# Kernel optimization log

Hardware: AMD Instinct MI355X
Metric: run time of the kernel (lower is better)

Reference implementation:

```python
import jax, jax.numpy as jnp
import numpy as np

V_NODES = 50000


def _spmm(vals, rows, cols, m):
    # sparse (V,V) @ dense (V, F): gather source rows, scale, scatter-add to dest rows
    return jax.ops.segment_sum(vals[:, None] * m[cols], rows, num_segments=V_NODES)


def setup_inputs() -> dict:
    key = jax.random.key(0)
    ks = jax.random.split(key, 6)
    B, Cin, Cout, K, V, E = 4, 128, 128, 5, V_NODES, 800000
    x = jax.random.normal(ks[0], (B, Cin, V), dtype=jnp.float32)
    # random symmetric-normalized-laplacian-like values (scaled so recurrence stays bounded)
    lap_vals = jax.random.normal(ks[1], (E,), dtype=jnp.float32) * 0.05
    fan_in = Cin  # kaiming_normal_ mode='fan_in' on (K, Cin, Cout): fan_in = Cin
    weight = jax.random.normal(ks[2], (K, Cin, Cout), dtype=jnp.float32) * np.sqrt(2.0 / fan_in)
    bias = jnp.full((Cout,), 0.01, dtype=jnp.float32)
    lap_rows = jax.random.randint(ks[3], (E,), 0, V, dtype=jnp.int32)
    lap_cols = jax.random.randint(ks[4], (E,), 0, V, dtype=jnp.int32)
    return {"x": x, "lap_vals": lap_vals, "weight": weight, "bias": bias,
            "lap_rows": lap_rows, "lap_cols": lap_cols}


def reference(x, lap_vals, weight, bias, lap_rows, lap_cols):
    B, Cin, V = x.shape
    K, _, Cout = weight.shape
    # (B, Cin, V) -> (V, B*Cin)
    x0 = jnp.transpose(x, (2, 0, 1)).reshape(V, B * Cin)

    def contract(xk, k):
        # accumulate order-k contribution: (V, B, Cin) x (Cin, Cout) -> (V, B, Cout)
        return jnp.einsum('vbi,io->vbo', xk.reshape(V, B, Cin), weight[k])

    out = contract(x0, 0)
    if K > 1:
        x1 = _spmm(lap_vals, lap_rows, lap_cols, x0)
        out = out + contract(x1, 1)
        for k in range(2, K):
            x2 = 2.0 * _spmm(lap_vals, lap_rows, lap_cols, x1) - x0
            out = out + contract(x2, k)
            x0, x1 = x1, x2
    out = out + bias  # broadcast over (V, B, Cout)
    # (V, B, Cout) -> (B, Cout, V)
    return jnp.transpose(out, (1, 2, 0))
```

## Files before the change

### kernel.cpp

```cpp
#include <hip/hip_runtime.h>

#define V_NODES 50000
#define FDIM    512
#define CIN     128
#define COUT    128
#define BATCH   4
#define KORD    5
#define KTOT    (KORD * CIN)
#define SCAN_NBLK ((V_NODES + 255) / 256)
#define TR_BLOCKS (((V_NODES + 63) / 64) * (FDIM / 64))
#define CONVW_BLOCKS ((KORD * COUT + 3) / 4)
#define QUANT_BLOCKS ((V_NODES + 3) / 4)

typedef short s16x8 __attribute__((ext_vector_type(8)));
typedef float f32x4 __attribute__((ext_vector_type(4)));
typedef int   i32x4 __attribute__((ext_vector_type(4)));

struct EPair { float w; int c; };

__device__ __forceinline__ float bf2f(unsigned short u) {
    union { unsigned int i; float f; } x; x.i = ((unsigned int)u) << 16; return x.f;
}
__device__ __forceinline__ unsigned short f2bf(float f) {
    union { float f; unsigned int i; } x; x.f = f;
    unsigned int r = x.i + 0x7fffu + ((x.i >> 16) & 1u);
    return (unsigned short)(r >> 16);
}

__global__ __launch_bounds__(256) void prep1_kernel(const float* __restrict__ x,
                                                    unsigned short* __restrict__ t0,
                                                    const int* __restrict__ rows,
                                                    int* __restrict__ cnt,
                                                    int E, int histBlocks,
                                                    const float* __restrict__ W,
                                                    signed char* __restrict__ Wq8,
                                                    float* __restrict__ Wsc) {
    __shared__ float tile[64][65];
    const int bid = blockIdx.x;
    if (bid < TR_BLOCKS) {
        const int v0 = (bid % ((V_NODES + 63) / 64)) * 64;
        const int r0 = (bid / ((V_NODES + 63) / 64)) * 64;
        const int lane = threadIdx.x & 63;
        const int w = threadIdx.x >> 6;
        #pragma unroll
        for (int i = 0; i < 16; ++i) {
            int rr = w * 16 + i;
            int v = v0 + lane;
            tile[rr][lane] = (v < V_NODES) ? x[(size_t)(r0 + rr) * V_NODES + v] : 0.0f;
        }
        __syncthreads();
        #pragma unroll
        for (int i = 0; i < 16; ++i) {
            int vv = w * 16 + i;
            int v = v0 + vv;
            if (v < V_NODES) t0[(size_t)v * FDIM + r0 + lane] = f2bf(tile[lane][vv]);
        }
    } else if (bid < TR_BLOCKS + histBlocks) {
        int e = (bid - TR_BLOCKS) * 256 + threadIdx.x;
        if (e < E) atomicAdd(&cnt[rows[e]], 1);
    } else {
        const int g = (bid - TR_BLOCKS - histBlocks) * 4 + (threadIdx.x >> 6);
        if (g >= KORD * COUT) return;
        const int co = g & 127;
        const int ord = g >> 7;
        const int lane = threadIdx.x & 63;
        float w0 = W[(size_t)(ord * 128 + lane * 2 + 0) * COUT + co];
        float w1 = W[(size_t)(ord * 128 + lane * 2 + 1) * COUT + co];
        float m = fmaxf(fabsf(w0), fabsf(w1));
        #pragma unroll
        for (int off = 1; off < 64; off <<= 1) m = fmaxf(m, __shfl_xor(m, off, 64));
        float inv = (m > 0.f) ? 127.f / m : 0.f;
        int q0 = max(-127, min(127, (int)rintf(w0 * inv)));
        int q1 = max(-127, min(127, (int)rintf(w1 * inv)));
        unsigned short pk = (unsigned short)((q0 & 0xff) | ((q1 & 0xff) << 8));
        *(unsigned short*)(Wq8 + (size_t)co * KTOT + ord * 128 + lane * 2) = pk;
        if (lane == 0) Wsc[ord * 128 + co] = m / 127.f;
    }
}

__global__ __launch_bounds__(256) void scan1_kernel(const int* __restrict__ cnt,
                                                    int* __restrict__ rowPtr,
                                                    int* __restrict__ blkSum) {
    __shared__ int sh[256];
    const int t = threadIdx.x;
    const int i = blockIdx.x * 256 + t;
    int v = (i < V_NODES) ? cnt[i] : 0;
    sh[t] = v;
    __syncthreads();
    #pragma unroll
    for (int off = 1; off < 256; off <<= 1) {
        int u = (t >= off) ? sh[t - off] : 0;
        __syncthreads();
        sh[t] += u;
        __syncthreads();
    }
    if (i < V_NODES) rowPtr[i] = sh[t] - v;
    if (t == 255) blkSum[blockIdx.x] = sh[255];
}

__global__ __launch_bounds__(256) void scan23_kernel(const int* __restrict__ blkSum,
                                                     int* __restrict__ rowPtr,
                                                     int* __restrict__ cursor) {
    __shared__ int sh[256];
    const int t = threadIdx.x;
    int v = (t < SCAN_NBLK) ? blkSum[t] : 0;
    sh[t] = v;
    __syncthreads();
    #pragma unroll
    for (int off = 1; off < 256; off <<= 1) {
        int u = (t >= off) ? sh[t - off] : 0;
        __syncthreads();
        sh[t] += u;
        __syncthreads();
    }
    const int boff = sh[blockIdx.x] - blkSum[blockIdx.x];
    const int i = blockIdx.x * 256 + t;
    if (i < V_NODES) {
        int r = rowPtr[i] + boff;
        rowPtr[i] = r;
        cursor[i] = r;
    }
    if (blockIdx.x == 0 && t == 255) rowPtr[V_NODES] = sh[255];
}

__global__ __launch_bounds__(256) void prep2_kernel(const unsigned short* __restrict__ xb,
                                                    signed char* __restrict__ xi,
                                                    float* __restrict__ xs,
                                                    const float* __restrict__ vals,
                                                    const int* __restrict__ rows,
                                                    const int* __restrict__ cols,
                                                    int* __restrict__ cursor,
                                                    EPair* __restrict__ ep, int E) {
    const int bid = blockIdx.x;
    if (bid < QUANT_BLOCKS) {
        const int wid = threadIdx.x >> 6;
        const int lane = threadIdx.x & 63;
        const int row = bid * 4 + wid;
        if (row >= V_NODES) return;
        uint4 q = ((const uint4*)xb)[(size_t)row * 64 + lane];
        unsigned int u[4] = {q.x, q.y, q.z, q.w};
        float f[8];
        #pragma unroll
        for (int j = 0; j < 4; ++j) {
            f[2*j+0] = bf2f((unsigned short)(u[j] & 0xffffu));
            f[2*j+1] = bf2f((unsigned short)(u[j] >> 16));
        }
        float m = 0.f;
        #pragma unroll
        for (int j = 0; j < 8; ++j) m = fmaxf(m, fabsf(f[j]));
        #pragma unroll
        for (int off = 1; off < 64; off <<= 1) m = fmaxf(m, __shfl_xor(m, off, 64));
        float inv = (m > 0.f) ? 127.f / m : 0.f;
        uint2 o; unsigned int ow[2] = {0u, 0u};
        #pragma unroll
        for (int j = 0; j < 8; ++j) {
            int si = (int)rintf(f[j] * inv);
            si = max(-127, min(127, si));
            ow[j >> 2] |= ((unsigned int)(si & 0xff)) << (8 * (j & 3));
        }
        o.x = ow[0]; o.y = ow[1];
        ((uint2*)xi)[(size_t)row * 64 + lane] = o;
        if (lane == 0) xs[row] = m / 127.f;
    } else {
        int e = (bid - QUANT_BLOCKS) * 256 + threadIdx.x;
        if (e >= E) return;
        int r = rows[e];
        int pos = atomicAdd(&cursor[r], 1);
        EPair p; p.w = vals[e]; p.c = cols[e];
        ep[pos] = p;
    }
}

__global__ __launch_bounds__(256) void spmm_i8_kernel(const EPair* __restrict__ ep,
                                                      const int* __restrict__ rowPtr,
                                                      const signed char* __restrict__ xi,
                                                      const float* __restrict__ xsc,
                                                      const signed char* __restrict__ oldi,
                                                      const float* __restrict__ oldsc,
                                                      signed char* __restrict__ yi,
                                                      float* __restrict__ ysc,
                                                      float alpha, int beta) {
    const int wid = threadIdx.x >> 6;
    const int lane = threadIdx.x & 63;
    const int row = blockIdx.x * 4 + wid;
    if (row >= V_NODES) return;
    const int s = rowPtr[row], e_end = rowPtr[row + 1];
    const uint2* __restrict__ xq = (const uint2*)xi;

    float acc[8];
    #pragma unroll
    for (int j = 0; j < 8; ++j) acc[j] = 0.f;

    int e = s;
    for (; e + 3 < e_end; e += 4) {
        EPair p[4];
        #pragma unroll
        for (int i = 0; i < 4; ++i) p[i] = ep[e + i];
        float w[4];
        #pragma unroll
        for (int i = 0; i < 4; ++i) w[i] = p[i].w * xsc[p[i].c];
        uint2 q[4];
        #pragma unroll
        for (int i = 0; i < 4; ++i) q[i] = xq[(size_t)p[i].c * 64 + lane];
        #pragma unroll
        for (int i = 0; i < 4; ++i) {
            #pragma unroll
            for (int wd = 0; wd < 2; ++wd) {
                unsigned int uu = wd ? q[i].y : q[i].x;
                #pragma unroll
                for (int b = 0; b < 4; ++b) {
                    float xv = (float)((signed char)(uu >> (8 * b)));
                    acc[wd * 4 + b] += w[i] * xv;
                }
            }
        }
    }
    for (; e < e_end; ++e) {
        EPair p0 = ep[e];
        float w0 = p0.w * xsc[p0.c];
        uint2 q0 = xq[(size_t)p0.c * 64 + lane];
        #pragma unroll
        for (int wd = 0; wd < 2; ++wd) {
            unsigned int uu = wd ? q0.y : q0.x;
            #pragma unroll
            for (int b = 0; b < 4; ++b) {
                float xv = (float)((signed char)(uu >> (8 * b)));
                acc[wd * 4 + b] += w0 * xv;
            }
        }
    }

    float r[8];
    #pragma unroll
    for (int j = 0; j < 8; ++j) r[j] = alpha * acc[j];
    if (beta) {
        uint2 q = ((const uint2*)oldi)[(size_t)row * 64 + lane];
        const float os = oldsc[row];
        #pragma unroll
        for (int wd = 0; wd < 2; ++wd) {
            unsigned int uu = wd ? q.y : q.x;
            #pragma unroll
            for (int b = 0; b < 4; ++b)
                r[wd * 4 + b] -= os * (float)((signed char)(uu >> (8 * b)));
        }
    }

    float m = 0.f;
    #pragma unroll
    for (int j = 0; j < 8; ++j) m = fmaxf(m, fabsf(r[j]));
    #pragma unroll
    for (int off = 1; off < 64; off <<= 1) m = fmaxf(m, __shfl_xor(m, off, 64));
    float inv = (m > 0.f) ? 127.f / m : 0.f;
    unsigned int ow[2] = {0u, 0u};
    #pragma unroll
    for (int j = 0; j < 8; ++j) {
        int si = (int)rintf(r[j] * inv);
        si = max(-127, min(127, si));
        ow[j >> 2] |= ((unsigned int)(si & 0xff)) << (8 * (j & 3));
    }
    uint2 oi; oi.x = ow[0]; oi.y = ow[1];
    ((uint2*)yi)[(size_t)row * 64 + lane] = oi;
    if (lane == 0) ysc[row] = m / 127.f;
}

__global__ __launch_bounds__(512) void gemm_mfma_kernel(const signed char* __restrict__ Ti8,
                                                        const float* __restrict__ Tsc,
                                                        const signed char* __restrict__ Wq8,
                                                        const float* __restrict__ Wsc,
                                                        const float* __restrict__ bias,
                                                        float* __restrict__ out) {
    __shared__ signed char Abuf[3][128 * 64];
    const int tid = threadIdx.x;
    const int lane = tid & 63;
    const int wid = tid >> 6;
    const int wr = wid >> 2;
    const int wc = wid & 3;
    const int v0 = blockIdx.x * 128;
    const int b = blockIdx.y;
    const int lr = lane & 15;
    const int lk = lane >> 4;

    size_t gof;
    {
        int rl = tid >> 2;
        int ch = tid & 3;
        int rowg = v0 + rl;
        if (rowg >= V_NODES) rowg = V_NODES - 1;
        int srcch = (ch - ((rl >> 1) & 3)) & 3;
        gof = (size_t)rowg * FDIM + b * CIN + (size_t)(srcch << 4);
    }

    f32x4 accF[4][2];
    i32x4 accI[4][2];
    #pragma unroll
    for (int mf = 0; mf < 4; ++mf)
        #pragma unroll
        for (int nf = 0; nf < 2; ++nf) {
            accF[mf][nf] = (f32x4){0.f, 0.f, 0.f, 0.f};
            accI[mf][nf] = (i32x4){0, 0, 0, 0};
        }

    const signed char* Bb = Wq8 + (size_t)(wc * 32 + lr) * KTOT + lk * 16;

    #pragma unroll
    for (int st = 0; st < 2; ++st) {
        const size_t soff = (size_t)(st & 1) * 64;
        __builtin_amdgcn_global_load_lds(
            (const __attribute__((address_space(1))) void*)(Ti8 + gof + soff),
            (__attribute__((address_space(3))) void*)(&Abuf[st][tid * 16]),
            16, 0, 0);
    }
    i32x4 bcur[2];
    #pragma unroll
    for (int nf = 0; nf < 2; ++nf)
        bcur[nf] = *(const i32x4*)(Bb + (size_t)nf * 16 * KTOT);
    f32x4 sv[4];
    float swv0 = 0.f, swv1 = 0.f;
    asm volatile("s_waitcnt vmcnt(0)" ::: "memory");
    asm volatile("s_barrier" ::: "memory");

    int curm = 0, stm = 2;
    #pragma unroll 1
    for (int s = 0; s < 10; ++s) {
        i32x4 bnxt[2];
        if (s < 9) {
            #pragma unroll
            for (int nf = 0; nf < 2; ++nf)
                bnxt[nf] = *(const i32x4*)(Bb + (size_t)nf * 16 * KTOT + (s + 1) * 64);
        }
        if (!(s & 1)) {
            const int ord = s >> 1;
            #pragma unroll
            for (int mf = 0; mf < 4; ++mf) {
                int base = v0 + wr * 64 + mf * 16 + lk * 4;
                if (base > V_NODES - 4) base = V_NODES - 4;
                sv[mf] = *(const f32x4*)(Tsc + (size_t)ord * V_NODES + base);
            }
            swv0 = Wsc[ord * 128 + wc * 32 + lr];
            swv1 = Wsc[ord * 128 + wc * 32 + 16 + lr];
        }
        __builtin_amdgcn_sched_barrier(0);
        if (s < 8) {
            const int sn = s + 2;
            const size_t soff = (size_t)(sn >> 1) * ((size_t)V_NODES * FDIM) + (size_t)((sn & 1) * 64);
            __builtin_amdgcn_global_load_lds(
                (const __attribute__((address_space(1))) void*)(Ti8 + gof + soff),
                (__attribute__((address_space(3))) void*)(&Abuf[stm][tid * 16]),
                16, 0, 0);
        }
        const signed char* Ab = &Abuf[curm][0];
        i32x4 a[4];
        #pragma unroll
        for (int mf = 0; mf < 4; ++mf) {
            int rl = wr * 64 + mf * 16 + lr;
            int phys = rl * 64 + (((lk + (rl >> 1)) & 3) << 4);
            a[mf] = *(const i32x4*)(Ab + phys);
        }
        #pragma unroll
        for (int mf = 0; mf < 4; ++mf)
            #pragma unroll
            for (int nf = 0; nf < 2; ++nf)
                accI[mf][nf] = __builtin_amdgcn_mfma_i32_16x16x64_i8(a[mf], bcur[nf], accI[mf][nf], 0, 0, 0);
        if (s & 1) {
            #pragma unroll
            for (int mf = 0; mf < 4; ++mf)
                #pragma unroll
                for (int nf = 0; nf < 2; ++nf) {
                    float sw = nf ? swv1 : swv0;
                    #pragma unroll
                    for (int e = 0; e < 4; ++e)
                        accF[mf][nf][e] += (float)accI[mf][nf][e] * (sv[mf][e] * sw);
                    accI[mf][nf] = (i32x4){0, 0, 0, 0};
                }
        }
        if (s < 9) {
            bcur[0] = bnxt[0];
            bcur[1] = bnxt[1];
        }
        asm volatile("s_barrier" ::: "memory");
        curm = (curm == 2) ? 0 : curm + 1;
        stm  = (stm == 2) ? 0 : stm + 1;
    }

    float* lds_f = (float*)&Abuf[0][0];
    const float bs0 = bias[wc * 32 + lr];
    const float bs1 = bias[wc * 32 + 16 + lr];
    #pragma unroll
    for (int p = 0; p < 4; ++p) {
        if (wc == p) {
            #pragma unroll
            for (int mf = 0; mf < 4; ++mf)
                #pragma unroll
                for (int nf = 0; nf < 2; ++nf) {
                    int co_l = nf * 16 + lr;
                    int vbase = wr * 64 + mf * 16 + lk * 4;
                    f32x4 val = accF[mf][nf];
                    float bs = nf ? bs1 : bs0;
                    val[0] += bs; val[1] += bs; val[2] += bs; val[3] += bs;
                    *(f32x4*)(lds_f + co_l * 132 + vbase) = val;
                }
        }
        __syncthreads();
        #pragma unroll
        for (int i = 0; i < 2; ++i) {
            int flat = i * 512 + tid;
            int co_l = flat >> 5;
            int v4 = flat & 31;
            int v = v0 + v4 * 4;
            if (v < V_NODES) {
                f32x4 val = *(const f32x4*)(lds_f + co_l * 132 + v4 * 4);
                *(f32x4*)(out + (size_t)(b * COUT + p * 32 + co_l) * V_NODES + v) = val;
            }
        }
        __syncthreads();
    }
}

extern "C" void kernel_launch(void* const* d_in, const int* in_sizes, int n_in,
                              void* d_out, int out_size, void* d_ws, size_t ws_size,
                              hipStream_t stream) {
    const float* x    = (const float*)d_in[0];
    const float* vals = (const float*)d_in[1];
    const float* W    = (const float*)d_in[2];
    const float* bias = (const float*)d_in[3];
    const int* rows   = (const int*)d_in[4];
    const int* cols   = (const int*)d_in[5];
    const int E = in_sizes[1];
    float* out = (float*)d_out;

    unsigned short* T0bf = (unsigned short*)d_ws;
    signed char* i8T = (signed char*)(T0bf + (size_t)V_NODES * FDIM);
    float* sc  = (float*)(i8T + (size_t)KORD * V_NODES * FDIM);
    signed char* Wq8 = (signed char*)(sc + (size_t)KORD * V_NODES + 64);
    float* Wsc = (float*)(Wq8 + (size_t)COUT * KTOT);
    EPair* ep     = (EPair*)(Wsc + KORD * COUT);
    int*   rowPtr = (int*)(ep + E);
    int*   cursor = rowPtr + V_NODES + 1;
    int*   cnt    = cursor + V_NODES;
    int*   blkSum = cnt + V_NODES;

    signed char* i8T0 = i8T;
    signed char* i8T1 = i8T + 1 * (size_t)V_NODES * FDIM;
    signed char* i8T2 = i8T + 2 * (size_t)V_NODES * FDIM;
    signed char* i8T3 = i8T + 3 * (size_t)V_NODES * FDIM;
    signed char* i8T4 = i8T + 4 * (size_t)V_NODES * FDIM;
    float* sc0 = sc + 0 * (size_t)V_NODES;
    float* sc1 = sc + 1 * (size_t)V_NODES;
    float* sc2 = sc + 2 * (size_t)V_NODES;
    float* sc3 = sc + 3 * (size_t)V_NODES;
    float* sc4 = sc + 4 * (size_t)V_NODES;

    const int histBlocks = (E + 255) / 256;
    const int spB4 = (V_NODES + 3) / 4;

    hipMemsetAsync(cnt, 0, V_NODES * sizeof(int), stream);
    prep1_kernel<<<TR_BLOCKS + histBlocks + CONVW_BLOCKS, 256, 0, stream>>>(
        x, T0bf, rows, cnt, E, histBlocks, W, Wq8, Wsc);
    scan1_kernel<<<SCAN_NBLK, 256, 0, stream>>>(cnt, rowPtr, blkSum);
    scan23_kernel<<<SCAN_NBLK, 256, 0, stream>>>(blkSum, rowPtr, cursor);
    prep2_kernel<<<QUANT_BLOCKS + histBlocks, 256, 0, stream>>>(
        T0bf, i8T0, sc0, vals, rows, cols, cursor, ep, E);

    spmm_i8_kernel<<<spB4, 256, 0, stream>>>(ep, rowPtr, i8T0, sc0, i8T0, sc0, i8T1, sc1, 1.f, 0);
    spmm_i8_kernel<<<spB4, 256, 0, stream>>>(ep, rowPtr, i8T1, sc1, i8T0, sc0, i8T2, sc2, 2.f, 1);
    spmm_i8_kernel<<<spB4, 256, 0, stream>>>(ep, rowPtr, i8T2, sc2, i8T1, sc1, i8T3, sc3, 2.f, 1);
    spmm_i8_kernel<<<spB4, 256, 0, stream>>>(ep, rowPtr, i8T3, sc3, i8T2, sc2, i8T4, sc4, 2.f, 1);

    dim3 gg((V_NODES + 127) / 128, BATCH);
    gemm_mfma_kernel<<<gg, 512, 0, stream>>>(i8T, sc, Wq8, Wsc, bias, out);
}
```

Measured before the change: 489.0 us.

## Quantize input directly to int8 without the bf16 transposed intermediate

Drops the bf16 transposed copy of the input. The first pass now reads the input column-wise to compute a per-node absmax scale. The second pass reads fp32 input again, quantizes with that scale, and transposes through LDS straight into the int8 layout. This cuts the bf16 write and re-read traffic, at the cost of reading the fp32 input twice and a strided per-node scan for the scale. Quantization now works from fp32 values rather than bf16-rounded ones, which changes rounding slightly.

```diff
diff --git a/kernel.cpp b/kernel.cpp
--- a/kernel.cpp
+++ b/kernel.cpp
@@ -8,58 +8,45 @@
 #define KORD    5
 #define KTOT    (KORD * CIN)
 #define SCAN_NBLK ((V_NODES + 255) / 256)
-#define TR_BLOCKS (((V_NODES + 63) / 64) * (FDIM / 64))
+#define VBLKS   ((V_NODES + 255) / 256)
+#define TQ_BLOCKS (VBLKS * (FDIM / 64))
 #define CONVW_BLOCKS ((KORD * COUT + 3) / 4)
-#define QUANT_BLOCKS ((V_NODES + 3) / 4)
-
-typedef short s16x8 __attribute__((ext_vector_type(8)));
+
 typedef float f32x4 __attribute__((ext_vector_type(4)));
 typedef int   i32x4 __attribute__((ext_vector_type(4)));
 
 struct EPair { float w; int c; };
 
-__device__ __forceinline__ float bf2f(unsigned short u) {
-    union { unsigned int i; float f; } x; x.i = ((unsigned int)u) << 16; return x.f;
-}
-__device__ __forceinline__ unsigned short f2bf(float f) {
-    union { float f; unsigned int i; } x; x.f = f;
-    unsigned int r = x.i + 0x7fffu + ((x.i >> 16) & 1u);
-    return (unsigned short)(r >> 16);
-}
-
 __global__ __launch_bounds__(256) void prep1_kernel(const float* __restrict__ x,
-                                                    unsigned short* __restrict__ t0,
+                                                    float* __restrict__ sc0,
+                                                    float* __restrict__ invsc,
                                                     const int* __restrict__ rows,
                                                     int* __restrict__ cnt,
                                                     int E, int histBlocks,
                                                     const float* __restrict__ W,
                                                     signed char* __restrict__ Wq8,
                                                     float* __restrict__ Wsc) {
-    __shared__ float tile[64][65];
     const int bid = blockIdx.x;
-    if (bid < TR_BLOCKS) {
-        const int v0 = (bid % ((V_NODES + 63) / 64)) * 64;
-        const int r0 = (bid / ((V_NODES + 63) / 64)) * 64;
-        const int lane = threadIdx.x & 63;
-        const int w = threadIdx.x >> 6;
-        #pragma unroll
-        for (int i = 0; i < 16; ++i) {
-            int rr = w * 16 + i;
-            int v = v0 + lane;
-            tile[rr][lane] = (v < V_NODES) ? x[(size_t)(r0 + rr) * V_NODES + v] : 0.0f;
-        }
-        __syncthreads();
-        #pragma unroll
-        for (int i = 0; i < 16; ++i) {
-            int vv = w * 16 + i;
-            int v = v0 + vv;
-            if (v < V_NODES) t0[(size_t)v * FDIM + r0 + lane] = f2bf(tile[lane][vv]);
-        }
-    } else if (bid < TR_BLOCKS + histBlocks) {
-        int e = (bid - TR_BLOCKS) * 256 + threadIdx.x;
+    if (bid < VBLKS) {
+        const int v = bid * 256 + threadIdx.x;
+        if (v >= V_NODES) return;
+        const float* xp = x + v;
+        float m0 = 0.f, m1 = 0.f, m2 = 0.f, m3 = 0.f;
+        #pragma unroll 4
+        for (int r = 0; r < FDIM; r += 4) {
+            m0 = fmaxf(m0, fabsf(xp[(size_t)(r + 0) * V_NODES]));
+            m1 = fmaxf(m1, fabsf(xp[(size_t)(r + 1) * V_NODES]));
+            m2 = fmaxf(m2, fabsf(xp[(size_t)(r + 2) * V_NODES]));
+            m3 = fmaxf(m3, fabsf(xp[(size_t)(r + 3) * V_NODES]));
+        }
+        float m = fmaxf(fmaxf(m0, m1), fmaxf(m2, m3));
+        sc0[v] = m / 127.f;
+        invsc[v] = (m > 0.f) ? 127.f / m : 0.f;
+    } else if (bid < VBLKS + histBlocks) {
+        int e = (bid - VBLKS) * 256 + threadIdx.x;
         if (e < E) atomicAdd(&cnt[rows[e]], 1);
     } else {
-        const int g = (bid - TR_BLOCKS - histBlocks) * 4 + (threadIdx.x >> 6);
+        const int g = (bid - VBLKS - histBlocks) * 4 + (threadIdx.x >> 6);
         if (g >= KORD * COUT) return;
         const int co = g & 127;
         const int ord = g >> 7;
@@ -123,46 +110,50 @@
     if (blockIdx.x == 0 && t == 255) rowPtr[V_NODES] = sh[255];
 }
 
-__global__ __launch_bounds__(256) void prep2_kernel(const unsigned short* __restrict__ xb,
+__global__ __launch_bounds__(256) void prep2_kernel(const float* __restrict__ x,
+                                                    const float* __restrict__ invsc,
                                                     signed char* __restrict__ xi,
-                                                    float* __restrict__ xs,
                                                     const float* __restrict__ vals,
                                                     const int* __restrict__ rows,
                                                     const int* __restrict__ cols,
                                                     int* __restrict__ cursor,
                                                     EPair* __restrict__ ep, int E) {
+    __shared__ signed char lds[256 * 80];
     const int bid = blockIdx.x;
-    if (bid < QUANT_BLOCKS) {
-        const int wid = threadIdx.x >> 6;
-        const int lane = threadIdx.x & 63;
-        const int row = bid * 4 + wid;
-        if (row >= V_NODES) return;
-        uint4 q = ((const uint4*)xb)[(size_t)row * 64 + lane];
-        unsigned int u[4] = {q.x, q.y, q.z, q.w};
-        float f[8];
-        #pragma unroll
-        for (int j = 0; j < 4; ++j) {
-            f[2*j+0] = bf2f((unsigned short)(u[j] & 0xffffu));
-            f[2*j+1] = bf2f((unsigned short)(u[j] >> 16));
-        }
-        float m = 0.f;
-        #pragma unroll
-        for (int j = 0; j < 8; ++j) m = fmaxf(m, fabsf(f[j]));
-        #pragma unroll
-        for (int off = 1; off < 64; off <<= 1) m = fmaxf(m, __shfl_xor(m, off, 64));
-        float inv = (m > 0.f) ? 127.f / m : 0.f;
-        uint2 o; unsigned int ow[2] = {0u, 0u};
-        #pragma unroll
-        for (int j = 0; j < 8; ++j) {
-            int si = (int)rintf(f[j] * inv);
-            si = max(-127, min(127, si));
-            ow[j >> 2] |= ((unsigned int)(si & 0xff)) << (8 * (j & 3));
-        }
-        o.x = ow[0]; o.y = ow[1];
-        ((uint2*)xi)[(size_t)row * 64 + lane] = o;
-        if (lane == 0) xs[row] = m / 127.f;
+    if (bid < TQ_BLOCKS) {
+        const int vb = bid % VBLKS;
+        const int rb = bid / VBLKS;
+        const int v0 = vb * 256, r0 = rb * 64;
+        const int t = threadIdx.x;
+        const int lane = t & 63, w = t >> 6;
+        int vbase = v0 + lane * 4;
+        if (vbase > V_NODES - 4) vbase = V_NODES - 4;
+        const f32x4 inv = *(const f32x4*)(invsc + vbase);
+        const int vv = lane * 4;
+        #pragma unroll
+        for (int i = 0; i < 16; ++i) {
+            const int r = r0 + w * 16 + i;
+            f32x4 xv = *(const f32x4*)(x + (size_t)r * V_NODES + vbase);
+            #pragma unroll
+            for (int j = 0; j < 4; ++j) {
+                int q = (int)rintf(xv[j] * inv[j]);
+                q = max(-127, min(127, q));
+                lds[(vv + j) * 80 + w * 16 + i] = (signed char)q;
+            }
+        }
+        __syncthreads();
+        #pragma unroll
+        for (int it = 0; it < 4; ++it) {
+            int flat = it * 256 + t;
+            int vl = flat >> 2, c = flat & 3;
+            int v = v0 + vl;
+            if (v < V_NODES) {
+                uint4 val = *(const uint4*)(lds + vl * 80 + c * 16);
+                *(uint4*)(xi + (size_t)v * FDIM + r0 + c * 16) = val;
+            }
+        }
     } else {
-        int e = (bid - QUANT_BLOCKS) * 256 + threadIdx.x;
+        int e = (bid - TQ_BLOCKS) * 256 + threadIdx.x;
         if (e >= E) return;
         int r = rows[e];
         int pos = atomicAdd(&cursor[r], 1);
@@ -428,10 +419,10 @@
     const int E = in_sizes[1];
     float* out = (float*)d_out;
 
-    unsigned short* T0bf = (unsigned short*)d_ws;
-    signed char* i8T = (signed char*)(T0bf + (size_t)V_NODES * FDIM);
+    signed char* i8T = (signed char*)d_ws;
     float* sc  = (float*)(i8T + (size_t)KORD * V_NODES * FDIM);
-    signed char* Wq8 = (signed char*)(sc + (size_t)KORD * V_NODES + 64);
+    float* invsc = sc + (size_t)KORD * V_NODES + 64;
+    signed char* Wq8 = (signed char*)(invsc + V_NODES + 64);
     float* Wsc = (float*)(Wq8 + (size_t)COUT * KTOT);
     EPair* ep     = (EPair*)(Wsc + KORD * COUT);
     int*   rowPtr = (int*)(ep + E);
@@ -454,12 +445,12 @@
     const int spB4 = (V_NODES + 3) / 4;
 
     hipMemsetAsync(cnt, 0, V_NODES * sizeof(int), stream);
-    prep1_kernel<<<TR_BLOCKS + histBlocks + CONVW_BLOCKS, 256, 0, stream>>>(
-        x, T0bf, rows, cnt, E, histBlocks, W, Wq8, Wsc);
+    prep1_kernel<<<VBLKS + histBlocks + CONVW_BLOCKS, 256, 0, stream>>>(
+        x, sc0, invsc, rows, cnt, E, histBlocks, W, Wq8, Wsc);
     scan1_kernel<<<SCAN_NBLK, 256, 0, stream>>>(cnt, rowPtr, blkSum);
     scan23_kernel<<<SCAN_NBLK, 256, 0, stream>>>(blkSum, rowPtr, cursor);
-    prep2_kernel<<<QUANT_BLOCKS + histBlocks, 256, 0, stream>>>(
-        T0bf, i8T0, sc0, vals, rows, cols, cursor, ep, E);
+    prep2_kernel<<<TQ_BLOCKS + histBlocks, 256, 0, stream>>>(
+        x, invsc, i8T0, vals, rows, cols, cursor, ep, E);
 
     spmm_i8_kernel<<<spB4, 256, 0, stream>>>(ep, rowPtr, i8T0, sc0, i8T0, sc0, i8T1, sc1, 1.f, 0);
     spmm_i8_kernel<<<spB4, 256, 0, stream>>>(ep, rowPtr, i8T1, sc1, i8T0, sc0, i8T2, sc2, 2.f, 1);
```

New measurement: 492.2 us. Within noise of the previous version (+0.7%).
